# Kernel optimization log

Hardware: AMD Instinct MI355X
Metric: run time of the kernel (lower is better)

## Reference

```python
import jax, jax.numpy as jnp
import numpy as np

INPUT_DIM = 1024
OUTPUT_DIM = 1024
NUM_SEGMENTS = 8
GRID_LO, GRID_HI = -1.0, 1.0


def setup_inputs() -> dict:
    key = jax.random.key(0)
    k1, k2 = jax.random.split(key)
    x = jax.random.normal(k1, (8, 2048, INPUT_DIM), dtype=jnp.float32)
    coeff = jax.random.normal(k2, (NUM_SEGMENTS + 1, OUTPUT_DIM, INPUT_DIM), dtype=jnp.float32) * 0.1
    bias = jnp.zeros((OUTPUT_DIM,), dtype=jnp.float32)
    return {"x": x, "coeff": coeff, "bias": bias}


def reference(x, coeff, bias):
    # x: (..., I); coeff: (G, O, I) with G = num_segments + 1; bias: (O,)
    batch_shape = x.shape[:-1]
    x_flat = x.reshape(-1, INPUT_DIM)                      # (B, I)
    grid = jnp.linspace(GRID_LO, GRID_HI, NUM_SEGMENTS + 1, dtype=x.dtype)  # (G,)
    h = (GRID_HI - GRID_LO) / NUM_SEGMENTS

    x_mean = jnp.mean(x_flat, axis=-1, keepdims=True)      # (B, 1)
    diff = x_mean - grid[None, :]                          # (B, G)
    w = jax.nn.relu(1.0 - jnp.abs(diff) / h)               # triangular hat weights
    w = w / (jnp.sum(w, axis=-1, keepdims=True) + 1e-8)    # (B, G)

    # Fused contraction order: avoid the (B, O, I) intermediate of the
    # original einsum chain; same math by associativity.
    t = jnp.einsum('bi,goi->bgo', x_flat, coeff)           # (B, G, O)
    out = jnp.einsum('bg,bgo->bo', w, t) + bias            # (B, O)
    return out.reshape(*batch_shape, OUTPUT_DIM)
```

## Files before the change

### kernel.cpp

```cpp
#include <hip/hip_runtime.h>
#include <math.h>

#define B_ROWS 16384
#define IDIM   1024
#define ODIM   1024
#define NGRID  9

#define RS_BLOCKS 1024
#define RS_ROWS   (B_ROWS / RS_BLOCKS)

#define GEMM_GROUPS 18
#define GEMM_BLOCKS (GEMM_GROUPS * 128)

typedef __attribute__((ext_vector_type(8))) short frag8;
typedef __attribute__((ext_vector_type(4))) float f32x4;

typedef __attribute__((address_space(1))) void gvoid;
typedef __attribute__((address_space(3))) void lvoid;

__device__ __forceinline__ void async_cp16(const void* g, void* l) {
  __builtin_amdgcn_global_load_lds((gvoid*)(void*)g, (lvoid*)l, 16, 0, 0);
}

__device__ __forceinline__ unsigned short f2bf(float f) {
  union { float f; unsigned u; } v; v.f = f;
  unsigned u = v.u;
  u += 0x7fffu + ((u >> 16) & 1u);
  return (unsigned short)(u >> 16);
}

__device__ __forceinline__ void seg_weights(float m, int& sI, float& w0, float& w1) {
  float wsum = 0.f, wg[NGRID];
#pragma unroll
  for (int g = 0; g < NGRID; g++) {
    float gv = -1.f + 0.25f * (float)g;
    float t = 1.f - fabsf(m - gv) * 4.f;
    wg[g] = t > 0.f ? t : 0.f;
    wsum += wg[g];
  }
  int s = (int)floorf((m + 1.f) * 4.f);
  s = s < 0 ? 0 : (s > 7 ? 7 : s);
  float inv = 1.f / (wsum + 1e-8f);
  sI = s;
  w0 = wg[s] * inv;
  w1 = wg[s + 1] * inv;
}

__global__ void zero_meta(int* bucket_cnt) {
  if (threadIdx.x < NGRID) bucket_cnt[threadIdx.x] = 0;
}

__global__ void row_stats_fused(const float* __restrict__ x,
                                unsigned short* __restrict__ Xb,
                                float2* __restrict__ ws2,
                                int* __restrict__ seg_rows,
                                int* __restrict__ bucket_cnt) {
  __shared__ int lcnt[NGRID];
  __shared__ int base[NGRID];
  __shared__ int lrank[RS_ROWS];
  __shared__ int lseg[RS_ROWS];
  const int tid  = threadIdx.x;
  const int lane = tid & 63;
  const int wave = tid >> 6;
  if (tid < NGRID) lcnt[tid] = 0;
  __syncthreads();
  const int row0 = blockIdx.x * RS_ROWS;
#pragma unroll
  for (int it = 0; it < RS_ROWS / 4; ++it) {
    int r = it * 4 + wave;
    int b = row0 + r;
    const float4* xr = (const float4*)(x + (size_t)b * IDIM);
    ushort4* xw = (ushort4*)(Xb + (size_t)b * IDIM);
    float4 v[4];
    float s = 0.f;
#pragma unroll
    for (int j = 0; j < 4; j++) {
      v[j] = xr[lane + j * 64];
      s += v[j].x + v[j].y + v[j].z + v[j].w;
    }
#pragma unroll
    for (int j = 0; j < 4; j++) {
      ushort4 u;
      u.x = f2bf(v[j].x); u.y = f2bf(v[j].y); u.z = f2bf(v[j].z); u.w = f2bf(v[j].w);
      xw[lane + j * 64] = u;
    }
#pragma unroll
    for (int off = 32; off; off >>= 1) s += __shfl_down(s, off, 64);
    if (lane == 0) {
      float m = s * (1.0f / (float)IDIM);
      int sI; float w0, w1;
      seg_weights(m, sI, w0, w1);
      ws2[b] = make_float2(w0, w1);
      lseg[r] = sI;
      lrank[r] = atomicAdd(&lcnt[sI], 1);
    }
  }
  __syncthreads();
  if (tid < NGRID) base[tid] = lcnt[tid] ? atomicAdd(&bucket_cnt[tid], lcnt[tid]) : 0;
  __syncthreads();
  if (tid < RS_ROWS)
    seg_rows[lseg[tid] * B_ROWS + base[lseg[tid]] + lrank[tid]] = row0 + tid;
}

#define CV_BLKS_PER_PLANE (ODIM * IDIM / 4 / 256)
__global__ void cvt_coeff(const float* __restrict__ c, unsigned short* __restrict__ cb,
                          const int* __restrict__ bucket_cnt) {
  const int g  = blockIdx.x >> 10;
  const int cI = blockIdx.x & 1023;
  bool need = bucket_cnt[g] > 0;
  if (!need && g > 0) need = bucket_cnt[g - 1] > 0;
  if (!need) return;
  int i = (g * CV_BLKS_PER_PLANE + cI) * 256 + threadIdx.x;
  float4 v = ((const float4*)c)[i];
  ushort4 o;
  o.x = f2bf(v.x); o.y = f2bf(v.y); o.z = f2bf(v.z); o.w = f2bf(v.w);
  ((ushort4*)cb)[i] = o;
}

__global__ void __launch_bounds__(256, 4)
kan_gemm(const unsigned short* __restrict__ Xb,
         const unsigned short* __restrict__ Cb,
         const int* __restrict__ seg_rows,
         const int* __restrict__ bucket_cnt,
         const float2* __restrict__ ws2,
         const float* __restrict__ bias,
         float* __restrict__ out) {
  const int sub = blockIdx.x & 127;
  const int mt  = (blockIdx.x >> 7) * 8 + (sub & 7);
  const int nt  = sub >> 3;

  int seg = -1, lt = 0, cnt = 0;
  {
    int t0 = 0;
#pragma unroll
    for (int g = 0; g < NGRID; g++) {
      int c   = bucket_cnt[g];
      int ntg = (c + 127) >> 7;
      if (mt >= t0 && mt < t0 + ntg) { seg = g; lt = mt - t0; cnt = c; }
      t0 += ntg;
    }
  }
  if (seg < 0) return;
  const int rlim = cnt - lt * 128;
  const int* rows = seg_rows + seg * B_ROWS + lt * 128;

  __shared__ unsigned short As[2][128 * 32];
  __shared__ unsigned short Bs0[2][64 * 32];
  __shared__ unsigned short Bs1[2][64 * 32];

  const int tid  = threadIdx.x;
  const int lane = tid & 63;
  const int wave = tid >> 6;
  const int wm   = wave >> 1;
  const int wn   = wave & 1;
  const int colB0 = nt * 64;

  const int lrow = lane >> 2;
  const int lswz = (((lane & 3) ^ ((lane >> 3) & 3))) * 8;
  const int rswz = (((lane >> 4) ^ ((lane >> 1) & 3))) * 8;

  int rid[2];
#pragma unroll
  for (int t = 0; t < 2; t++) {
    int idx = (wave * 2 + t) * 16 + lrow;
    rid[t] = rows[idx < rlim ? idx : rlim - 1];
  }

  const unsigned short* gB0 = Cb + ((size_t)(seg * ODIM + colB0 + wave * 16 + lrow)) * IDIM + lswz;
  const unsigned short* gB1 = gB0 + (size_t)ODIM * IDIM;

  f32x4 acc0[4][2] = {};
  f32x4 acc1[4][2] = {};

  for (int kk = 0; kk < IDIM; kk += 64) {
    __syncthreads();
#pragma unroll
    for (int h = 0; h < 2; h++) {
      int ko = kk + h * 32;
#pragma unroll
      for (int t = 0; t < 2; t++) {
        int r0 = (wave * 2 + t) * 16;
        async_cp16(Xb + (size_t)rid[t] * IDIM + ko + lswz, &As[h][r0 * 32]);
      }
      async_cp16(gB0 + ko, &Bs0[h][wave * 16 * 32]);
      async_cp16(gB1 + ko, &Bs1[h][wave * 16 * 32]);
    }
    __syncthreads();

#pragma unroll
    for (int h = 0; h < 2; h++) {
      frag8 af[4], bfr[2];
#pragma unroll
      for (int mi = 0; mi < 4; mi++)
        af[mi] = *(const frag8*)&As[h][(wm * 4 + mi) * 512 + (lane & 15) * 32 + rswz];
#pragma unroll
      for (int ni = 0; ni < 2; ni++)
        bfr[ni] = *(const frag8*)&Bs0[h][(wn * 2 + ni) * 512 + (lane & 15) * 32 + rswz];
#pragma unroll
      for (int mi = 0; mi < 4; mi++)
#pragma unroll
        for (int ni = 0; ni < 2; ni++)
          acc0[mi][ni] = __builtin_amdgcn_mfma_f32_16x16x32_bf16(af[mi], bfr[ni], acc0[mi][ni], 0, 0, 0);
#pragma unroll
      for (int ni = 0; ni < 2; ni++)
        bfr[ni] = *(const frag8*)&Bs1[h][(wn * 2 + ni) * 512 + (lane & 15) * 32 + rswz];
#pragma unroll
      for (int mi = 0; mi < 4; mi++)
#pragma unroll
        for (int ni = 0; ni < 2; ni++)
          acc1[mi][ni] = __builtin_amdgcn_mfma_f32_16x16x32_bf16(af[mi], bfr[ni], acc1[mi][ni], 0, 0, 0);
    }
  }

  int   col[2]; float bv[2];
#pragma unroll
  for (int ni = 0; ni < 2; ni++) {
    col[ni] = colB0 + wn * 32 + ni * 16 + (lane & 15);
    bv[ni]  = bias[col[ni]];
  }
#pragma unroll
  for (int mi = 0; mi < 4; mi++) {
    int irow = wm * 64 + mi * 16 + (lane >> 4) * 4;
#pragma unroll
    for (int r = 0; r < 4; r++) {
      int idx = irow + r;
      if (idx < rlim) {
        int orow = rows[idx];
        float2 w = ws2[orow];
        float* o = out + (size_t)orow * ODIM;
#pragma unroll
        for (int ni = 0; ni < 2; ni++)
          o[col[ni]] = w.x * acc0[mi][ni][r] + w.y * acc1[mi][ni][r] + bv[ni];
      }
    }
  }
}

__global__ void fallback_kernel(const float* __restrict__ x, const float* __restrict__ coeff,
                                const float* __restrict__ bias, float* __restrict__ out) {
  int b = blockIdx.x;
  int tid = threadIdx.x;
  __shared__ float xs[IDIM];
  __shared__ float ps[4];
  __shared__ float mw[2];
  __shared__ int   ms;
  float4 v = ((const float4*)(x + (size_t)b * IDIM))[tid];
  ((float4*)xs)[tid] = v;
  float s = v.x + v.y + v.z + v.w;
#pragma unroll
  for (int off = 32; off; off >>= 1) s += __shfl_down(s, off, 64);
  if ((tid & 63) == 0) ps[tid >> 6] = s;
  __syncthreads();
  if (tid == 0) {
    float m = (ps[0] + ps[1] + ps[2] + ps[3]) * (1.0f / (float)IDIM);
    int sI; float w0, w1;
    seg_weights(m, sI, w0, w1);
    mw[0] = w0; mw[1] = w1; ms = sI;
  }
  __syncthreads();
  float w0 = mw[0], w1 = mw[1]; int sI = ms;
  for (int o = tid; o < ODIM; o += 256) {
    const float* c0 = coeff + ((size_t)sI * ODIM + o) * IDIM;
    const float* c1 = c0 + (size_t)ODIM * IDIM;
    float a0 = 0.f, a1 = 0.f;
    for (int i = 0; i < IDIM; i++) { a0 += xs[i] * c0[i]; a1 += xs[i] * c1[i]; }
    out[(size_t)b * ODIM + o] = w0 * a0 + w1 * a1 + bias[o];
  }
}

extern "C" void kernel_launch(void* const* d_in, const int* in_sizes, int n_in,
                              void* d_out, int out_size, void* d_ws, size_t ws_size,
                              hipStream_t stream) {
  const float* x     = (const float*)d_in[0];
  const float* coeff = (const float*)d_in[1];
  const float* bias  = (const float*)d_in[2];
  float* out = (float*)d_out;

  size_t szXb = (size_t)B_ROWS * IDIM * sizeof(unsigned short);
  size_t szCb = (size_t)NGRID * ODIM * IDIM * sizeof(unsigned short);
  size_t o0 = 0;
  unsigned short* Xb = (unsigned short*)((char*)d_ws + o0); o0 += szXb;
  unsigned short* Cb = (unsigned short*)((char*)d_ws + o0); o0 += szCb;
  float2* ws2 = (float2*)((char*)d_ws + o0); o0 += (size_t)B_ROWS * 8;
  int* seg_rows = (int*)((char*)d_ws + o0); o0 += (size_t)NGRID * B_ROWS * 4;
  int* bucket_cnt = (int*)((char*)d_ws + o0); o0 += 256;

  if (ws_size < o0) {
    fallback_kernel<<<B_ROWS, 256, 0, stream>>>(x, coeff, bias, out);
    return;
  }

  zero_meta<<<1, 64, 0, stream>>>(bucket_cnt);
  row_stats_fused<<<RS_BLOCKS, 256, 0, stream>>>(x, Xb, ws2, seg_rows, bucket_cnt);
  cvt_coeff<<<NGRID * CV_BLKS_PER_PLANE, 256, 0, stream>>>(coeff, Cb, bucket_cnt);
  kan_gemm<<<GEMM_BLOCKS, 256, 0, stream>>>(Xb, Cb, seg_rows, bucket_cnt, ws2, bias, out);
}
```

Measured before the change: 231.5 us.

## Enlarge GEMM tiles to 256x128 with 512 threads and a double-buffered async pipeline

Result: slower. 324.7 us (+40.2%).

```diff
diff --git a/kernel.cpp b/kernel.cpp
--- a/kernel.cpp
+++ b/kernel.cpp
@@ -9,8 +9,9 @@
 #define RS_BLOCKS 1024
 #define RS_ROWS   (B_ROWS / RS_BLOCKS)
 
-#define GEMM_GROUPS 18
-#define GEMM_BLOCKS (GEMM_GROUPS * 128)
+#define GEMM_MSLOTS 80
+#define GEMM_NT     8
+#define GEMM_BLOCKS (GEMM_MSLOTS * GEMM_NT)
 
 typedef __attribute__((ext_vector_type(8))) short frag8;
 typedef __attribute__((ext_vector_type(4))) float f32x4;
@@ -44,10 +45,6 @@
   sI = s;
   w0 = wg[s] * inv;
   w1 = wg[s + 1] * inv;
-}
-
-__global__ void zero_meta(int* bucket_cnt) {
-  if (threadIdx.x < NGRID) bucket_cnt[threadIdx.x] = 0;
 }
 
 __global__ void row_stats_fused(const float* __restrict__ x,
@@ -117,7 +114,7 @@
   ((ushort4*)cb)[i] = o;
 }
 
-__global__ void __launch_bounds__(256, 4)
+__global__ void __launch_bounds__(512, 2)
 kan_gemm(const unsigned short* __restrict__ Xb,
          const unsigned short* __restrict__ Cb,
          const int* __restrict__ seg_rows,
@@ -125,8 +122,8 @@
          const float2* __restrict__ ws2,
          const float* __restrict__ bias,
          float* __restrict__ out) {
-  const int sub = blockIdx.x & 127;
-  const int mt  = (blockIdx.x >> 7) * 8 + (sub & 7);
+  const int sub = blockIdx.x & 63;
+  const int mt  = (blockIdx.x >> 6) * 8 + (sub & 7);
   const int nt  = sub >> 3;
 
   int seg = -1, lt = 0, cnt = 0;
@@ -135,82 +132,100 @@
 #pragma unroll
     for (int g = 0; g < NGRID; g++) {
       int c   = bucket_cnt[g];
-      int ntg = (c + 127) >> 7;
+      int ntg = (c + 255) >> 8;
       if (mt >= t0 && mt < t0 + ntg) { seg = g; lt = mt - t0; cnt = c; }
       t0 += ntg;
     }
   }
   if (seg < 0) return;
-  const int rlim = cnt - lt * 128;
-  const int* rows = seg_rows + seg * B_ROWS + lt * 128;
-
-  __shared__ unsigned short As[2][128 * 32];
-  __shared__ unsigned short Bs0[2][64 * 32];
-  __shared__ unsigned short Bs1[2][64 * 32];
+  const int rlim = cnt - lt * 256;
+  const int* rows = seg_rows + seg * B_ROWS + lt * 256;
+
+  __shared__ unsigned short As[2][256 * 64];
+  __shared__ unsigned short Bs[2][256 * 64];
 
   const int tid  = threadIdx.x;
   const int lane = tid & 63;
   const int wave = tid >> 6;
-  const int wm   = wave >> 1;
-  const int wn   = wave & 1;
-  const int colB0 = nt * 64;
-
-  const int lrow = lane >> 2;
-  const int lswz = (((lane & 3) ^ ((lane >> 3) & 3))) * 8;
-  const int rswz = (((lane >> 4) ^ ((lane >> 1) & 3))) * 8;
-
-  int rid[2];
-#pragma unroll
-  for (int t = 0; t < 2; t++) {
-    int idx = (wave * 2 + t) * 16 + lrow;
-    rid[t] = rows[idx < rlim ? idx : rlim - 1];
-  }
-
-  const unsigned short* gB0 = Cb + ((size_t)(seg * ODIM + colB0 + wave * 16 + lrow)) * IDIM + lswz;
-  const unsigned short* gB1 = gB0 + (size_t)ODIM * IDIM;
-
-  f32x4 acc0[4][2] = {};
-  f32x4 acc1[4][2] = {};
-
-  for (int kk = 0; kk < IDIM; kk += 64) {
-    __syncthreads();
-#pragma unroll
-    for (int h = 0; h < 2; h++) {
-      int ko = kk + h * 32;
-#pragma unroll
-      for (int t = 0; t < 2; t++) {
-        int r0 = (wave * 2 + t) * 16;
-        async_cp16(Xb + (size_t)rid[t] * IDIM + ko + lswz, &As[h][r0 * 32]);
-      }
-      async_cp16(gB0 + ko, &Bs0[h][wave * 16 * 32]);
-      async_cp16(gB1 + ko, &Bs1[h][wave * 16 * 32]);
-    }
-    __syncthreads();
-
-#pragma unroll
-    for (int h = 0; h < 2; h++) {
-      frag8 af[4], bfr[2];
-#pragma unroll
-      for (int mi = 0; mi < 4; mi++)
-        af[mi] = *(const frag8*)&As[h][(wm * 4 + mi) * 512 + (lane & 15) * 32 + rswz];
-#pragma unroll
-      for (int ni = 0; ni < 2; ni++)
-        bfr[ni] = *(const frag8*)&Bs0[h][(wn * 2 + ni) * 512 + (lane & 15) * 32 + rswz];
-#pragma unroll
-      for (int mi = 0; mi < 4; mi++)
-#pragma unroll
-        for (int ni = 0; ni < 2; ni++)
-          acc0[mi][ni] = __builtin_amdgcn_mfma_f32_16x16x32_bf16(af[mi], bfr[ni], acc0[mi][ni], 0, 0, 0);
-#pragma unroll
-      for (int ni = 0; ni < 2; ni++)
-        bfr[ni] = *(const frag8*)&Bs1[h][(wn * 2 + ni) * 512 + (lane & 15) * 32 + rswz];
-#pragma unroll
-      for (int mi = 0; mi < 4; mi++)
-#pragma unroll
-        for (int ni = 0; ni < 2; ni++)
-          acc1[mi][ni] = __builtin_amdgcn_mfma_f32_16x16x32_bf16(af[mi], bfr[ni], acc1[mi][ni], 0, 0, 0);
-    }
-  }
+  const int wm   = wave >> 2;
+  const int wn   = wave & 3;
+  const int colB0 = nt * 128;
+
+  const int sgrow  = wave * 8 + (lane >> 3);
+  const int schunk = ((lane & 7) ^ ((lane >> 3) & 7)) * 8;
+
+  int rid[4];
+#pragma unroll
+  for (int i = 0; i < 4; i++) {
+    int idx = i * 64 + sgrow;
+    rid[i] = rows[idx < rlim ? idx : rlim - 1];
+  }
+  const unsigned short* gA[4];
+  const unsigned short* gB[4];
+#pragma unroll
+  for (int i = 0; i < 4; i++) {
+    gA[i] = Xb + (size_t)rid[i] * IDIM + schunk;
+    int s = i * 64 + sgrow;
+    gB[i] = Cb + ((size_t)((seg + (s >> 7)) * ODIM + colB0 + (s & 127))) * IDIM + schunk;
+  }
+
+  const int arow = wm * 128 + (lane & 15);
+  const int brow = wn * 32 + (lane & 15);
+  const int cs0  = (((lane >> 4) + 0) ^ (lane & 7)) * 8;
+  const int cs1  = (((lane >> 4) + 4) ^ (lane & 7)) * 8;
+
+  f32x4 acc[2][8][2] = {};
+
+#define STAGE(buf, kk) do {                                                   \
+    _Pragma("unroll")                                                         \
+    for (int i = 0; i < 4; i++)                                               \
+      async_cp16(gA[i] + (kk), &As[buf][(i * 64 + wave * 8) * 64]);           \
+    _Pragma("unroll")                                                         \
+    for (int i = 0; i < 4; i++)                                               \
+      async_cp16(gB[i] + (kk), &Bs[buf][(i * 64 + wave * 8) * 64]);           \
+  } while (0)
+
+#define HALF(buf, CS) do {                                                    \
+    frag8 af[8]; frag8 bf[2][2];                                              \
+    _Pragma("unroll")                                                         \
+    for (int mi = 0; mi < 8; mi++)                                            \
+      af[mi] = *(const frag8*)&As[buf][(arow + mi * 16) * 64 + (CS)];         \
+    _Pragma("unroll")                                                         \
+    for (int p = 0; p < 2; p++)                                               \
+      _Pragma("unroll")                                                       \
+      for (int ni = 0; ni < 2; ni++)                                          \
+        bf[p][ni] = *(const frag8*)&Bs[buf][(brow + p * 128 + ni * 16) * 64 + (CS)]; \
+    __builtin_amdgcn_s_setprio(1);                                            \
+    _Pragma("unroll")                                                         \
+    for (int mi = 0; mi < 8; mi++)                                            \
+      _Pragma("unroll")                                                       \
+      for (int p = 0; p < 2; p++)                                             \
+        _Pragma("unroll")                                                     \
+        for (int ni = 0; ni < 2; ni++)                                        \
+          acc[p][mi][ni] = __builtin_amdgcn_mfma_f32_16x16x32_bf16(           \
+              af[mi], bf[p][ni], acc[p][mi][ni], 0, 0, 0);                    \
+    __builtin_amdgcn_s_setprio(0);                                            \
+  } while (0)
+
+  STAGE(0, 0);
+  STAGE(1, 64);
+
+#pragma unroll 2
+  for (int t = 0; t < 16; ++t) {
+    const int cur = t & 1;
+    if (t < 15) asm volatile("s_waitcnt vmcnt(8)" ::: "memory");
+    else        asm volatile("s_waitcnt vmcnt(0)" ::: "memory");
+    __builtin_amdgcn_s_barrier();
+    __builtin_amdgcn_sched_barrier(0);
+    HALF(cur, cs0);
+    HALF(cur, cs1);
+    asm volatile("s_waitcnt lgkmcnt(0)" ::: "memory");
+    __builtin_amdgcn_sched_barrier(0);
+    __builtin_amdgcn_s_barrier();
+    if (t < 14) STAGE(cur, (t + 2) * 64);
+  }
+#undef STAGE
+#undef HALF
 
   int   col[2]; float bv[2];
 #pragma unroll
@@ -219,8 +234,8 @@
     bv[ni]  = bias[col[ni]];
   }
 #pragma unroll
-  for (int mi = 0; mi < 4; mi++) {
-    int irow = wm * 64 + mi * 16 + (lane >> 4) * 4;
+  for (int mi = 0; mi < 8; mi++) {
+    int irow = wm * 128 + mi * 16 + (lane >> 4) * 4;
 #pragma unroll
     for (int r = 0; r < 4; r++) {
       int idx = irow + r;
@@ -230,7 +245,7 @@
         float* o = out + (size_t)orow * ODIM;
 #pragma unroll
         for (int ni = 0; ni < 2; ni++)
-          o[col[ni]] = w.x * acc0[mi][ni][r] + w.y * acc1[mi][ni][r] + bv[ni];
+          o[col[ni]] = w.x * acc[0][mi][ni][r] + w.y * acc[1][mi][ni][r] + bv[ni];
       }
     }
   }
@@ -290,8 +305,8 @@
     return;
   }
 
-  zero_meta<<<1, 64, 0, stream>>>(bucket_cnt);
+  hipMemsetAsync(bucket_cnt, 0, NGRID * sizeof(int), stream);
   row_stats_fused<<<RS_BLOCKS, 256, 0, stream>>>(x, Xb, ws2, seg_rows, bucket_cnt);
   cvt_coeff<<<NGRID * CV_BLKS_PER_PLANE, 256, 0, stream>>>(coeff, Cb, bucket_cnt);
-  kan_gemm<<<GEMM_BLOCKS, 256, 0, stream>>>(Xb, Cb, seg_rows, bucket_cnt, ws2, bias, out);
-}
+  kan_gemm<<<GEMM_BLOCKS, 512, 0, stream>>>(Xb, Cb, seg_rows, bucket_cnt, ws2, bias, out);
+}
```

## Widen GEMM tile to 128 output columns with unified B buffer

Applied to the files above, without the earlier changes.

Measured after the change: 254.1 us. 1.1x slower.

```diff
diff --git a/kernel.cpp b/kernel.cpp
--- a/kernel.cpp
+++ b/kernel.cpp
@@ -9,8 +9,9 @@
 #define RS_BLOCKS 1024
 #define RS_ROWS   (B_ROWS / RS_BLOCKS)
 
-#define GEMM_GROUPS 18
-#define GEMM_BLOCKS (GEMM_GROUPS * 128)
+#define GEMM_MSLOTS 136
+#define GEMM_NT     8
+#define GEMM_BLOCKS ((GEMM_MSLOTS / 8) * 64)
 
 typedef __attribute__((ext_vector_type(8))) short frag8;
 typedef __attribute__((ext_vector_type(4))) float f32x4;
@@ -44,10 +45,6 @@
   sI = s;
   w0 = wg[s] * inv;
   w1 = wg[s + 1] * inv;
-}
-
-__global__ void zero_meta(int* bucket_cnt) {
-  if (threadIdx.x < NGRID) bucket_cnt[threadIdx.x] = 0;
 }
 
 __global__ void row_stats_fused(const float* __restrict__ x,
@@ -117,7 +114,7 @@
   ((ushort4*)cb)[i] = o;
 }
 
-__global__ void __launch_bounds__(256, 4)
+__global__ void __launch_bounds__(256, 2)
 kan_gemm(const unsigned short* __restrict__ Xb,
          const unsigned short* __restrict__ Cb,
          const int* __restrict__ seg_rows,
@@ -125,8 +122,8 @@
          const float2* __restrict__ ws2,
          const float* __restrict__ bias,
          float* __restrict__ out) {
-  const int sub = blockIdx.x & 127;
-  const int mt  = (blockIdx.x >> 7) * 8 + (sub & 7);
+  const int sub = blockIdx.x & 63;
+  const int mt  = (blockIdx.x >> 6) * 8 + (sub & 7);
   const int nt  = sub >> 3;
 
   int seg = -1, lt = 0, cnt = 0;
@@ -145,32 +142,34 @@
   const int* rows = seg_rows + seg * B_ROWS + lt * 128;
 
   __shared__ unsigned short As[2][128 * 32];
-  __shared__ unsigned short Bs0[2][64 * 32];
-  __shared__ unsigned short Bs1[2][64 * 32];
+  __shared__ unsigned short Bs[2][256 * 32];
 
   const int tid  = threadIdx.x;
   const int lane = tid & 63;
   const int wave = tid >> 6;
-  const int wm   = wave >> 1;
-  const int wn   = wave & 1;
-  const int colB0 = nt * 64;
-
-  const int lrow = lane >> 2;
-  const int lswz = (((lane & 3) ^ ((lane >> 3) & 3))) * 8;
+  const int wn   = wave;
+  const int colB0 = nt * 128;
+
+  const int srow16 = lane >> 2;
+  const int schunk = ((lane & 3) ^ ((lane >> 3) & 3)) * 8;
+
+  const unsigned short* gA[2];
+#pragma unroll
+  for (int i = 0; i < 2; i++) {
+    int idx = (wave * 2 + i) * 16 + srow16;
+    int rid = rows[idx < rlim ? idx : rlim - 1];
+    gA[i] = Xb + (size_t)rid * IDIM + schunk;
+  }
+  const unsigned short* gB[4];
+#pragma unroll
+  for (int i = 0; i < 4; i++) {
+    int e = (wave * 4 + i) * 16 + srow16;
+    gB[i] = Cb + ((size_t)((seg + (e >> 7)) * ODIM + colB0 + (e & 127))) * IDIM + schunk;
+  }
+
   const int rswz = (((lane >> 4) ^ ((lane >> 1) & 3))) * 8;
 
-  int rid[2];
-#pragma unroll
-  for (int t = 0; t < 2; t++) {
-    int idx = (wave * 2 + t) * 16 + lrow;
-    rid[t] = rows[idx < rlim ? idx : rlim - 1];
-  }
-
-  const unsigned short* gB0 = Cb + ((size_t)(seg * ODIM + colB0 + wave * 16 + lrow)) * IDIM + lswz;
-  const unsigned short* gB1 = gB0 + (size_t)ODIM * IDIM;
-
-  f32x4 acc0[4][2] = {};
-  f32x4 acc1[4][2] = {};
+  f32x4 acc[8][4] = {};
 
   for (int kk = 0; kk < IDIM; kk += 64) {
     __syncthreads();
@@ -178,49 +177,42 @@
     for (int h = 0; h < 2; h++) {
       int ko = kk + h * 32;
 #pragma unroll
-      for (int t = 0; t < 2; t++) {
-        int r0 = (wave * 2 + t) * 16;
-        async_cp16(Xb + (size_t)rid[t] * IDIM + ko + lswz, &As[h][r0 * 32]);
+      for (int i = 0; i < 2; i++)
+        async_cp16(gA[i] + ko, &As[h][(wave * 2 + i) * 512]);
+#pragma unroll
+      for (int i = 0; i < 4; i++)
+        async_cp16(gB[i] + ko, &Bs[h][(wave * 4 + i) * 512]);
+    }
+    __syncthreads();
+
+#pragma unroll
+    for (int h = 0; h < 2; h++) {
+      frag8 af[8], bfr[4];
+#pragma unroll
+      for (int mi = 0; mi < 8; mi++)
+        af[mi] = *(const frag8*)&As[h][(mi * 16 + (lane & 15)) * 32 + rswz];
+#pragma unroll
+      for (int ni = 0; ni < 4; ni++) {
+        int e = (ni >> 1) * 128 + wn * 32 + (ni & 1) * 16 + (lane & 15);
+        bfr[ni] = *(const frag8*)&Bs[h][e * 32 + rswz];
       }
-      async_cp16(gB0 + ko, &Bs0[h][wave * 16 * 32]);
-      async_cp16(gB1 + ko, &Bs1[h][wave * 16 * 32]);
-    }
-    __syncthreads();
-
-#pragma unroll
-    for (int h = 0; h < 2; h++) {
-      frag8 af[4], bfr[2];
-#pragma unroll
-      for (int mi = 0; mi < 4; mi++)
-        af[mi] = *(const frag8*)&As[h][(wm * 4 + mi) * 512 + (lane & 15) * 32 + rswz];
-#pragma unroll
-      for (int ni = 0; ni < 2; ni++)
-        bfr[ni] = *(const frag8*)&Bs0[h][(wn * 2 + ni) * 512 + (lane & 15) * 32 + rswz];
-#pragma unroll
-      for (int mi = 0; mi < 4; mi++)
-#pragma unroll
-        for (int ni = 0; ni < 2; ni++)
-          acc0[mi][ni] = __builtin_amdgcn_mfma_f32_16x16x32_bf16(af[mi], bfr[ni], acc0[mi][ni], 0, 0, 0);
-#pragma unroll
-      for (int ni = 0; ni < 2; ni++)
-        bfr[ni] = *(const frag8*)&Bs1[h][(wn * 2 + ni) * 512 + (lane & 15) * 32 + rswz];
-#pragma unroll
-      for (int mi = 0; mi < 4; mi++)
-#pragma unroll
-        for (int ni = 0; ni < 2; ni++)
-          acc1[mi][ni] = __builtin_amdgcn_mfma_f32_16x16x32_bf16(af[mi], bfr[ni], acc1[mi][ni], 0, 0, 0);
+#pragma unroll
+      for (int mi = 0; mi < 8; mi++)
+#pragma unroll
+        for (int ni = 0; ni < 4; ni++)
+          acc[mi][ni] = __builtin_amdgcn_mfma_f32_16x16x32_bf16(af[mi], bfr[ni], acc[mi][ni], 0, 0, 0);
     }
   }
 
   int   col[2]; float bv[2];
 #pragma unroll
-  for (int ni = 0; ni < 2; ni++) {
-    col[ni] = colB0 + wn * 32 + ni * 16 + (lane & 15);
-    bv[ni]  = bias[col[ni]];
-  }
-#pragma unroll
-  for (int mi = 0; mi < 4; mi++) {
-    int irow = wm * 64 + mi * 16 + (lane >> 4) * 4;
+  for (int nc = 0; nc < 2; nc++) {
+    col[nc] = colB0 + wn * 32 + nc * 16 + (lane & 15);
+    bv[nc]  = bias[col[nc]];
+  }
+#pragma unroll
+  for (int mi = 0; mi < 8; mi++) {
+    int irow = mi * 16 + (lane >> 4) * 4;
 #pragma unroll
     for (int r = 0; r < 4; r++) {
       int idx = irow + r;
@@ -229,8 +221,8 @@
         float2 w = ws2[orow];
         float* o = out + (size_t)orow * ODIM;
 #pragma unroll
-        for (int ni = 0; ni < 2; ni++)
-          o[col[ni]] = w.x * acc0[mi][ni][r] + w.y * acc1[mi][ni][r] + bv[ni];
+        for (int nc = 0; nc < 2; nc++)
+          o[col[nc]] = w.x * acc[mi][nc][r] + w.y * acc[mi][2 + nc][r] + bv[nc];
       }
     }
   }
@@ -290,7 +282,7 @@
     return;
   }
 
-  zero_meta<<<1, 64, 0, stream>>>(bucket_cnt);
+  hipMemsetAsync(bucket_cnt, 0, NGRID * sizeof(int), stream);
   row_stats_fused<<<RS_BLOCKS, 256, 0, stream>>>(x, Xb, ws2, seg_rows, bucket_cnt);
   cvt_coeff<<<NGRID * CV_BLKS_PER_PLANE, 256, 0, stream>>>(coeff, Cb, bucket_cnt);
   kan_gemm<<<GEMM_BLOCKS, 256, 0, stream>>>(Xb, Cb, seg_rows, bucket_cnt, ws2, bias, out);
```

## Use full-width 64-k LDS tiles with XOR swizzle and segment-sorted weights

Applied to the files above, without the earlier changes.

New measurement: 234.9 us. About the same (+1.5%).

```diff
diff --git a/kernel.cpp b/kernel.cpp
--- a/kernel.cpp
+++ b/kernel.cpp
@@ -46,19 +46,16 @@
   w1 = wg[s + 1] * inv;
 }
 
-__global__ void zero_meta(int* bucket_cnt) {
-  if (threadIdx.x < NGRID) bucket_cnt[threadIdx.x] = 0;
-}
-
 __global__ void row_stats_fused(const float* __restrict__ x,
                                 unsigned short* __restrict__ Xb,
-                                float2* __restrict__ ws2,
+                                float2* __restrict__ ws_s,
                                 int* __restrict__ seg_rows,
                                 int* __restrict__ bucket_cnt) {
   __shared__ int lcnt[NGRID];
   __shared__ int base[NGRID];
   __shared__ int lrank[RS_ROWS];
   __shared__ int lseg[RS_ROWS];
+  __shared__ float2 lws[RS_ROWS];
   const int tid  = threadIdx.x;
   const int lane = tid & 63;
   const int wave = tid >> 6;
@@ -90,7 +87,7 @@
       float m = s * (1.0f / (float)IDIM);
       int sI; float w0, w1;
       seg_weights(m, sI, w0, w1);
-      ws2[b] = make_float2(w0, w1);
+      lws[r] = make_float2(w0, w1);
       lseg[r] = sI;
       lrank[r] = atomicAdd(&lcnt[sI], 1);
     }
@@ -98,8 +95,11 @@
   __syncthreads();
   if (tid < NGRID) base[tid] = lcnt[tid] ? atomicAdd(&bucket_cnt[tid], lcnt[tid]) : 0;
   __syncthreads();
-  if (tid < RS_ROWS)
-    seg_rows[lseg[tid] * B_ROWS + base[lseg[tid]] + lrank[tid]] = row0 + tid;
+  if (tid < RS_ROWS) {
+    int p = lseg[tid] * B_ROWS + base[lseg[tid]] + lrank[tid];
+    seg_rows[p] = row0 + tid;
+    ws_s[p] = lws[tid];
+  }
 }
 
 #define CV_BLKS_PER_PLANE (ODIM * IDIM / 4 / 256)
@@ -122,7 +122,7 @@
          const unsigned short* __restrict__ Cb,
          const int* __restrict__ seg_rows,
          const int* __restrict__ bucket_cnt,
-         const float2* __restrict__ ws2,
+         const float2* __restrict__ ws_s,
          const float* __restrict__ bias,
          float* __restrict__ out) {
   const int sub = blockIdx.x & 127;
@@ -144,9 +144,9 @@
   const int rlim = cnt - lt * 128;
   const int* rows = seg_rows + seg * B_ROWS + lt * 128;
 
-  __shared__ unsigned short As[2][128 * 32];
-  __shared__ unsigned short Bs0[2][64 * 32];
-  __shared__ unsigned short Bs1[2][64 * 32];
+  __shared__ unsigned short As [128 * 64];
+  __shared__ unsigned short Bs0[ 64 * 64];
+  __shared__ unsigned short Bs1[ 64 * 64];
 
   const int tid  = threadIdx.x;
   const int lane = tid & 63;
@@ -155,19 +155,27 @@
   const int wn   = wave & 1;
   const int colB0 = nt * 64;
 
-  const int lrow = lane >> 2;
-  const int lswz = (((lane & 3) ^ ((lane >> 3) & 3))) * 8;
-  const int rswz = (((lane >> 4) ^ ((lane >> 1) & 3))) * 8;
-
-  int rid[2];
-#pragma unroll
-  for (int t = 0; t < 2; t++) {
-    int idx = (wave * 2 + t) * 16 + lrow;
-    rid[t] = rows[idx < rlim ? idx : rlim - 1];
-  }
-
-  const unsigned short* gB0 = Cb + ((size_t)(seg * ODIM + colB0 + wave * 16 + lrow)) * IDIM + lswz;
-  const unsigned short* gB1 = gB0 + (size_t)ODIM * IDIM;
+  const int srow = lane >> 3;
+  const int sOff = ((lane & 7) ^ srow) * 8;
+
+  const unsigned short* gA[4];
+#pragma unroll
+  for (int i = 0; i < 4; i++) {
+    int idx = (wave * 4 + i) * 8 + srow;
+    int rid = rows[idx < rlim ? idx : rlim - 1];
+    gA[i] = Xb + (size_t)rid * IDIM + sOff;
+  }
+  const unsigned short* gB0[2];
+  const unsigned short* gB1[2];
+#pragma unroll
+  for (int i = 0; i < 2; i++) {
+    int rr = wave * 16 + i * 8 + srow;
+    gB0[i] = Cb + ((size_t)(seg * ODIM + colB0 + rr)) * IDIM + sOff;
+    gB1[i] = gB0[i] + (size_t)ODIM * IDIM;
+  }
+
+  const int rsw0 = ((((lane >> 4) & 3) | 0) ^ (lane & 7)) * 8;
+  const int rsw1 = ((((lane >> 4) & 3) | 4) ^ (lane & 7)) * 8;
 
   f32x4 acc0[4][2] = {};
   f32x4 acc1[4][2] = {};
@@ -175,27 +183,25 @@
   for (int kk = 0; kk < IDIM; kk += 64) {
     __syncthreads();
 #pragma unroll
+    for (int i = 0; i < 4; i++)
+      async_cp16(gA[i] + kk, &As[(wave * 4 + i) * 512]);
+#pragma unroll
+    for (int i = 0; i < 2; i++) {
+      async_cp16(gB0[i] + kk, &Bs0[(wave * 2 + i) * 512]);
+      async_cp16(gB1[i] + kk, &Bs1[(wave * 2 + i) * 512]);
+    }
+    __syncthreads();
+
+#pragma unroll
     for (int h = 0; h < 2; h++) {
-      int ko = kk + h * 32;
-#pragma unroll
-      for (int t = 0; t < 2; t++) {
-        int r0 = (wave * 2 + t) * 16;
-        async_cp16(Xb + (size_t)rid[t] * IDIM + ko + lswz, &As[h][r0 * 32]);
-      }
-      async_cp16(gB0 + ko, &Bs0[h][wave * 16 * 32]);
-      async_cp16(gB1 + ko, &Bs1[h][wave * 16 * 32]);
-    }
-    __syncthreads();
-
-#pragma unroll
-    for (int h = 0; h < 2; h++) {
+      const int rs = h ? rsw1 : rsw0;
       frag8 af[4], bfr[2];
 #pragma unroll
       for (int mi = 0; mi < 4; mi++)
-        af[mi] = *(const frag8*)&As[h][(wm * 4 + mi) * 512 + (lane & 15) * 32 + rswz];
+        af[mi] = *(const frag8*)&As[(wm * 64 + mi * 16 + (lane & 15)) * 64 + rs];
 #pragma unroll
       for (int ni = 0; ni < 2; ni++)
-        bfr[ni] = *(const frag8*)&Bs0[h][(wn * 2 + ni) * 512 + (lane & 15) * 32 + rswz];
+        bfr[ni] = *(const frag8*)&Bs0[((wn * 2 + ni) * 16 + (lane & 15)) * 64 + rs];
 #pragma unroll
       for (int mi = 0; mi < 4; mi++)
 #pragma unroll
@@ -203,7 +209,7 @@
           acc0[mi][ni] = __builtin_amdgcn_mfma_f32_16x16x32_bf16(af[mi], bfr[ni], acc0[mi][ni], 0, 0, 0);
 #pragma unroll
       for (int ni = 0; ni < 2; ni++)
-        bfr[ni] = *(const frag8*)&Bs1[h][(wn * 2 + ni) * 512 + (lane & 15) * 32 + rswz];
+        bfr[ni] = *(const frag8*)&Bs1[((wn * 2 + ni) * 16 + (lane & 15)) * 64 + rs];
 #pragma unroll
       for (int mi = 0; mi < 4; mi++)
 #pragma unroll
@@ -212,6 +218,7 @@
     }
   }
 
+  const float2* wss = ws_s + seg * B_ROWS + lt * 128;
   int   col[2]; float bv[2];
 #pragma unroll
   for (int ni = 0; ni < 2; ni++) {
@@ -226,7 +233,7 @@
       int idx = irow + r;
       if (idx < rlim) {
         int orow = rows[idx];
-        float2 w = ws2[orow];
+        float2 w = wss[idx];
         float* o = out + (size_t)orow * ODIM;
 #pragma unroll
         for (int ni = 0; ni < 2; ni++)
@@ -281,7 +288,7 @@
   size_t o0 = 0;
   unsigned short* Xb = (unsigned short*)((char*)d_ws + o0); o0 += szXb;
   unsigned short* Cb = (unsigned short*)((char*)d_ws + o0); o0 += szCb;
-  float2* ws2 = (float2*)((char*)d_ws + o0); o0 += (size_t)B_ROWS * 8;
+  float2* ws_s = (float2*)((char*)d_ws + o0); o0 += (size_t)NGRID * B_ROWS * 8;
   int* seg_rows = (int*)((char*)d_ws + o0); o0 += (size_t)NGRID * B_ROWS * 4;
   int* bucket_cnt = (int*)((char*)d_ws + o0); o0 += 256;
 
@@ -290,8 +297,8 @@
     return;
   }
 
-  zero_meta<<<1, 64, 0, stream>>>(bucket_cnt);
-  row_stats_fused<<<RS_BLOCKS, 256, 0, stream>>>(x, Xb, ws2, seg_rows, bucket_cnt);
+  hipMemsetAsync(bucket_cnt, 0, NGRID * sizeof(int), stream);
+  row_stats_fused<<<RS_BLOCKS, 256, 0, stream>>>(x, Xb, ws_s, seg_rows, bucket_cnt);
   cvt_coeff<<<NGRID * CV_BLKS_PER_PLANE, 256, 0, stream>>>(coeff, Cb, bucket_cnt);
-  kan_gemm<<<GEMM_BLOCKS, 256, 0, stream>>>(Xb, Cb, seg_rows, bucket_cnt, ws2, bias, out);
-}
+  kan_gemm<<<GEMM_BLOCKS, 256, 0, stream>>>(Xb, Cb, seg_rows, bucket_cnt, ws_s, bias, out);
+}
```
